# Kernel tuning notes

Measured on AMD Instinct MI355X. Metric: run time of the kernel, lower is better.

Reference implementation:

```python
import jax, jax.numpy as jnp
import numpy as np

COF1 = 0.01
EPS = 1e-8  # matches F.cosine_similarity default eps


def setup_inputs() -> dict:
    key = jax.random.key(0)
    latent = jax.random.normal(key, (8192, 64), dtype=jnp.float32)
    return {"latent": latent}


def reference(latent):
    # rows whose elementwise sum is nonzero participate (as i and as j)
    mask = (jnp.sum(latent, axis=1) != 0).astype(latent.dtype)  # [N]
    # L2-normalize rows with eps clamp (cosine similarity denominator)
    norm = jnp.maximum(jnp.sqrt(jnp.sum(latent * latent, axis=1, keepdims=True)), EPS)
    ln = latent / norm  # [N, d]
    sim = ln @ ln.T  # [N, N] pairwise cosine similarities
    # sum over selected (i, j) pairs, minus 1 per selected row i (self-sim correction)
    total = jnp.einsum('i,ij,j->', mask, sim, mask) - jnp.sum(mask)
    n = latent.shape[0]
    return COF1 * total / (2.0 * n)
```

## Files before the change

kernel.cpp:

```cpp
#include <hip/hip_runtime.h>


#define EPSV 1e-8f
#define COF1 0.01f

constexpr int N_ROWS = 8192;
constexpr int DIM = 64;
constexpr int TPB = 256;
constexpr int WPB = TPB / 64;
constexpr int BLOCKS = 64;
constexpr int RPW = N_ROWS / (BLOCKS * WPB);
constexpr int SLOT = 68;

__global__ __launch_bounds__(TPB, 2) void cl_partial(const float* __restrict__ latent,
                                                     float* __restrict__ ws) {
    const int wv   = threadIdx.x >> 6;
    const int lane = threadIdx.x & 63;
    const int g    = lane >> 4;
    const int c4   = lane & 15;
    const int row0 = (blockIdx.x * WPB + wv) * RPW;

    const float4* lat4 = (const float4*)latent;

    float4 x[RPW / 4];
    #pragma unroll
    for (int b = 0; b < RPW / 4; ++b)
        x[b] = lat4[(row0 + b * 4 + g) * (DIM / 4) + c4];

    float4 v = make_float4(0.f, 0.f, 0.f, 0.f);
    float cnt = 0.0f;
    #pragma unroll
    for (int b = 0; b < RPW / 4; ++b) {
        float s = x[b].x + x[b].y + x[b].z + x[b].w;
        float q = x[b].x * x[b].x + x[b].y * x[b].y + x[b].z * x[b].z + x[b].w * x[b].w;
        #pragma unroll
        for (int off = 8; off; off >>= 1) {
            s += __shfl_xor(s, off);
            q += __shfl_xor(q, off);
        }
        if (s != 0.0f) {
            float inv = 1.0f / fmaxf(sqrtf(q), EPSV);
            v.x += x[b].x * inv; v.y += x[b].y * inv;
            v.z += x[b].z * inv; v.w += x[b].w * inv;
            if (c4 == 0) cnt += 1.0f;
        }
    }
    #pragma unroll
    for (int off = 16; off <= 32; off <<= 1) {
        v.x += __shfl_xor(v.x, off); v.y += __shfl_xor(v.y, off);
        v.z += __shfl_xor(v.z, off); v.w += __shfl_xor(v.w, off);
        cnt += __shfl_xor(cnt, off);
    }

    __shared__ float4 sv4[WPB][16];
    __shared__ float  scnt[WPB];
    if (lane < 16) sv4[wv][c4] = v;
    if (lane == 0) scnt[wv] = cnt;
    __syncthreads();

    if (wv == 0 && lane < 16) {
        float4 a = sv4[0][c4];
        float4 b1 = sv4[1][c4], b2 = sv4[2][c4], b3 = sv4[3][c4];
        a.x += b1.x + b2.x + b3.x; a.y += b1.y + b2.y + b3.y;
        a.z += b1.z + b2.z + b3.z; a.w += b1.w + b2.w + b3.w;
        ((float4*)(ws + blockIdx.x * SLOT))[c4] = a;
        if (lane == 0)
            ws[blockIdx.x * SLOT + 64] = scnt[0] + scnt[1] + scnt[2] + scnt[3];
    }
}

__global__ __launch_bounds__(64) void cl_final(const float* __restrict__ ws,
                                               float* __restrict__ out) {
    const int lane = threadIdx.x;
    const int g    = lane >> 4;
    const int c4   = lane & 15;
    const float4* ws4 = (const float4*)ws;

    float4 f[16];
    #pragma unroll
    for (int j = 0; j < 16; ++j)
        f[j] = ws4[(4 * j + g) * (SLOT / 4) + c4];
    float c = ws[lane * SLOT + 64];

    float4 vq = make_float4(0.f, 0.f, 0.f, 0.f);
    #pragma unroll
    for (int j = 0; j < 16; ++j) {
        vq.x += f[j].x; vq.y += f[j].y; vq.z += f[j].z; vq.w += f[j].w;
    }
    #pragma unroll
    for (int off = 16; off <= 32; off <<= 1) {
        vq.x += __shfl_xor(vq.x, off); vq.y += __shfl_xor(vq.y, off);
        vq.z += __shfl_xor(vq.z, off); vq.w += __shfl_xor(vq.w, off);
    }
    #pragma unroll
    for (int off = 32; off; off >>= 1)
        c += __shfl_xor(c, off);

    float d = vq.x * vq.x + vq.y * vq.y + vq.z * vq.z + vq.w * vq.w;
    #pragma unroll
    for (int off = 8; off; off >>= 1)
        d += __shfl_xor(d, off);

    if (lane == 0)
        out[0] = COF1 * (d - c) / (2.0f * (float)N_ROWS);
}

extern "C" void kernel_launch(void* const* d_in, const int* in_sizes, int n_in,
                              void* d_out, int out_size, void* d_ws, size_t ws_size,
                              hipStream_t stream) {
    const float* latent = (const float*)d_in[0];
    float* out = (float*)d_out;
    float* ws = (float*)d_ws;

    cl_partial<<<BLOCKS, TPB, 0, stream>>>(latent, ws);
    cl_final<<<1, 64, 0, stream>>>(ws, out);
}
```

Baseline: 12.21 us.

## Fuse partial and final reduction into one kernel using completion flags

```diff
diff --git a/kernel.cpp b/kernel.cpp
--- a/kernel.cpp
+++ b/kernel.cpp
@@ -8,12 +8,15 @@
 constexpr int DIM = 64;
 constexpr int TPB = 256;
 constexpr int WPB = TPB / 64;
-constexpr int BLOCKS = 64;
+constexpr int BLOCKS = 128;
 constexpr int RPW = N_ROWS / (BLOCKS * WPB);
 constexpr int SLOT = 68;
+constexpr unsigned MAGIC = 0x5EEDF00Du;
 
-__global__ __launch_bounds__(TPB, 2) void cl_partial(const float* __restrict__ latent,
-                                                     float* __restrict__ ws) {
+__global__ __launch_bounds__(TPB, 2) void cl_fused(const float* __restrict__ latent,
+                                                   float* __restrict__ ws,
+                                                   unsigned* __restrict__ flags,
+                                                   float* __restrict__ out) {
     const int wv   = threadIdx.x >> 6;
     const int lane = threadIdx.x & 63;
     const int g    = lane >> 4;
@@ -66,27 +69,40 @@
         ((float4*)(ws + blockIdx.x * SLOT))[c4] = a;
         if (lane == 0)
             ws[blockIdx.x * SLOT + 64] = scnt[0] + scnt[1] + scnt[2] + scnt[3];
+        __threadfence();
     }
-}
+    __syncthreads();
+    if (threadIdx.x == 0)
+        __hip_atomic_store(&flags[blockIdx.x], MAGIC,
+                           __ATOMIC_RELEASE, __HIP_MEMORY_SCOPE_AGENT);
+    __syncthreads();
 
-__global__ __launch_bounds__(64) void cl_final(const float* __restrict__ ws,
-                                               float* __restrict__ out) {
-    const int lane = threadIdx.x;
-    const int g    = lane >> 4;
-    const int c4   = lane & 15;
+    unsigned f = MAGIC;
+    if (threadIdx.x < BLOCKS)
+        f = __hip_atomic_load(&flags[threadIdx.x],
+                              __ATOMIC_RELAXED, __HIP_MEMORY_SCOPE_AGENT);
+    unsigned long long bal = __ballot(f == MAGIC);
+    __shared__ unsigned wok[WPB];
+    if (lane == 0) wok[wv] = (bal == ~0ull) ? 1u : 0u;
+    __syncthreads();
+    if (!(wok[0] & wok[1] & wok[2] & wok[3])) return;
+
+    __threadfence();
+
+    if (threadIdx.x >= 64 && threadIdx.x < 64 + BLOCKS)
+        flags[threadIdx.x - 64] = 0;
+
+    if (wv != 0) return;
+
     const float4* ws4 = (const float4*)ws;
-
-    float4 f[16];
-    #pragma unroll
-    for (int j = 0; j < 16; ++j)
-        f[j] = ws4[(4 * j + g) * (SLOT / 4) + c4];
-    float c = ws[lane * SLOT + 64];
-
     float4 vq = make_float4(0.f, 0.f, 0.f, 0.f);
     #pragma unroll
-    for (int j = 0; j < 16; ++j) {
-        vq.x += f[j].x; vq.y += f[j].y; vq.z += f[j].z; vq.w += f[j].w;
+    for (int j = 0; j < 32; ++j) {
+        float4 t = ws4[(4 * j + g) * (SLOT / 4) + c4];
+        vq.x += t.x; vq.y += t.y; vq.z += t.z; vq.w += t.w;
     }
+    float c = ws[lane * SLOT + 64] + ws[(64 + lane) * SLOT + 64];
+
     #pragma unroll
     for (int off = 16; off <= 32; off <<= 1) {
         vq.x += __shfl_xor(vq.x, off); vq.y += __shfl_xor(vq.y, off);
@@ -111,7 +127,7 @@
     const float* latent = (const float*)d_in[0];
     float* out = (float*)d_out;
     float* ws = (float*)d_ws;
+    unsigned* flags = (unsigned*)(ws + BLOCKS * SLOT);
 
-    cl_partial<<<BLOCKS, TPB, 0, stream>>>(latent, ws);
-    cl_final<<<1, 64, 0, stream>>>(ws, out);
+    cl_fused<<<BLOCKS, TPB, 0, stream>>>(latent, ws, flags, out);
 }
```

Result: slower. 17.82 us (+45.9%).
